# Optimization experiments

Measured on AMD Instinct MI355X. Metric: run time of the kernel, lower is better.

## Reference

```python
import jax, jax.numpy as jnp
import numpy as np

EMBED = 1024
HEADS = 16
HEAD_DIM = EMBED // HEADS
MLP = 4 * EMBED
EPS = 1e-6


def setup_inputs() -> dict:
    key = jax.random.key(0)
    ks = jax.random.split(key, 16)
    B, N, C = 2, 2048, EMBED
    x = jax.random.normal(ks[0], (B, N, C), dtype=jnp.float32)
    c = jax.random.normal(ks[1], (B, C), dtype=jnp.float32)
    attention_mask = jax.random.randint(ks[2], (B, N), 0, 2, dtype=jnp.int32)
    s = 0.02
    params = {
        "norm_w": jnp.ones((C,), jnp.float32),
        "scale_w": s * jax.random.normal(ks[3], (C, C), jnp.float32),
        "scale_b": s * jax.random.normal(ks[4], (C,), jnp.float32),
        "shift_w": s * jax.random.normal(ks[5], (C, C), jnp.float32),
        "shift_b": s * jax.random.normal(ks[6], (C,), jnp.float32),
        "qkv_w": s * jax.random.normal(ks[7], (3 * C, C), jnp.float32),
        "proj_w": s * jax.random.normal(ks[8], (C, C), jnp.float32),
        "proj_b": s * jax.random.normal(ks[9], (C,), jnp.float32),
        "mlp_w1": s * jax.random.normal(ks[10], (2 * MLP, C), jnp.float32),
        "mlp_b1": s * jax.random.normal(ks[11], (2 * MLP,), jnp.float32),
        "mlp_w2": s * jax.random.normal(ks[12], (C, MLP), jnp.float32),
        "mlp_b2": s * jax.random.normal(ks[13], (C,), jnp.float32),
    }
    return {"x": x, "c": c, "attention_mask": attention_mask, **params}


def _adaln(x, c, norm_w, scale_w, scale_b, shift_w, shift_b):
    sc = jax.nn.silu(c)
    shift = sc @ shift_w.T + shift_b                      # [B,C]
    scale = jnp.clip(sc @ scale_w.T + scale_b + 1.0, 0.1, 10.0)
    # RMSNorm: ||x|| * C^-0.5, clamped below by eps
    norm = jnp.maximum(jnp.linalg.norm(x, axis=-1, keepdims=True) * x.shape[-1] ** -0.5, EPS)
    h = x / norm * norm_w
    return h * scale[:, None, :] + shift[:, None, :]


def _attention(x, attention_mask, qkv_w, proj_w, proj_b):
    B, N, C = x.shape
    qkv = (x @ qkv_w.T).reshape(B, N, 3, HEADS, HEAD_DIM)
    q = qkv[:, :, 0].transpose(0, 2, 1, 3)  # [B,H,N,D]
    k = qkv[:, :, 1].transpose(0, 2, 1, 3)
    v = qkv[:, :, 2].transpose(0, 2, 1, 3)
    attn = jnp.einsum("bhnd,bhmd->bhnm", q, k) * (HEAD_DIM ** -0.5)
    mask = attention_mask[:, None, None, :]              # [B,1,1,N] over keys
    attn = jnp.where(mask == 0, -jnp.inf, attn)
    all_inf = jnp.all(attn == -jnp.inf, axis=-1, keepdims=True)
    attn = jnp.where(all_inf, 0.0, attn)
    p = jax.nn.softmax(attn, axis=-1)
    out = jnp.einsum("bhnm,bhmd->bhnd", p, v).transpose(0, 2, 1, 3).reshape(B, N, C)
    return out @ proj_w.T + proj_b


def _mlp(x, w1, b1, w2, b2):
    h = x @ w1.T + b1
    x1, x2 = jnp.split(h, 2, axis=-1)
    return (jax.nn.silu(x1) * x2) @ w2.T + b2


def reference(x, c, attention_mask, norm_w, scale_w, scale_b, shift_w, shift_b,
              qkv_w, proj_w, proj_b, mlp_w1, mlp_b1, mlp_w2, mlp_b2):
    x = x + _attention(_adaln(x, c, norm_w, scale_w, scale_b, shift_w, shift_b),
                       attention_mask, qkv_w, proj_w, proj_b)
    x = x + _mlp(_adaln(x, c, norm_w, scale_w, scale_b, shift_w, shift_b),
                 mlp_w1, mlp_b1, mlp_w2, mlp_b2)
    return x
```

## Files before the change

### kernel.cpp

```cpp
#include <hip/hip_runtime.h>
#include <cstdint>
#include <cstddef>

#define DEVINL __device__ __forceinline__

typedef __bf16 bf16x8 __attribute__((ext_vector_type(8)));
typedef float  f32x4  __attribute__((ext_vector_type(4)));


DEVINL unsigned short f2b(float f) {
  unsigned u = __builtin_bit_cast(unsigned, f);
  u += 0x7fffu + ((u >> 16) & 1u);
  return (unsigned short)(u >> 16);
}

DEVINL unsigned packtrunc(float a, float b) {
  unsigned ua = __builtin_bit_cast(unsigned, a);
  unsigned ub = __builtin_bit_cast(unsigned, b);
  return (ua >> 16) | (ub & 0xffff0000u);
}

DEVINL void async16(void* lds, const void* g) {
  __builtin_amdgcn_global_load_lds((const __attribute__((address_space(1))) unsigned*)g,
                                   (__attribute__((address_space(3))) unsigned*)lds,
                                   16, 0, 0);
}


__global__ void cvt4_kernel(const float* __restrict__ s0, const float* __restrict__ s1,
                            const float* __restrict__ s2, const float* __restrict__ s3,
                            unsigned short* __restrict__ d0, unsigned short* __restrict__ d1,
                            unsigned short* __restrict__ d2, unsigned short* __restrict__ d3) {
  int i = blockIdx.x * 256 + threadIdx.x;
  if (i < 786432) {
    float4 v = ((const float4*)s0)[i];
    ushort4 o; o.x = f2b(v.x); o.y = f2b(v.y); o.z = f2b(v.z); o.w = f2b(v.w);
    ((ushort4*)d0)[i] = o;
  } else if (i < 1048576) {
    int off = i - 786432;
    float4 v = ((const float4*)s1)[off];
    ushort4 o; o.x = f2b(v.x); o.y = f2b(v.y); o.z = f2b(v.z); o.w = f2b(v.w);
    ((ushort4*)d1)[off] = o;
  } else if (i < 3145728) {
    int off = i - 1048576;
    int row = off >> 8, col = off & 255;
    int rp = (row < 4096) ? (row << 1) : (((row - 4096) << 1) | 1);
    float4 v = ((const float4*)s2)[off];
    ushort4 o; o.x = f2b(v.x); o.y = f2b(v.y); o.z = f2b(v.z); o.w = f2b(v.w);
    ((ushort4*)d2)[rp * 256 + col] = o;
  } else {
    int off = i - 3145728;
    float4 v = ((const float4*)s3)[off];
    ushort4 o; o.x = f2b(v.x); o.y = f2b(v.y); o.z = f2b(v.z); o.w = f2b(v.w);
    ((ushort4*)d3)[off] = o;
  }
}


__global__ void cond_kernel(const float* __restrict__ c,
                            const float* __restrict__ scale_w, const float* __restrict__ scale_b,
                            const float* __restrict__ shift_w, const float* __restrict__ shift_b,
                            float* __restrict__ scale_o, float* __restrict__ shift_o) {
  __shared__ float sc[1024];
  __shared__ float red[2][4][64];
  int tid = threadIdx.x;
  int b = blockIdx.x >> 4, ch = blockIdx.x & 15;
  for (int i = tid; i < 1024; i += 256) {
    float cv = c[b * 1024 + i];
    sc[i] = cv / (1.f + __expf(-cv));
  }
  __syncthreads();
  int colidx = tid & 63, p = tid >> 6;
  int co = ch * 64 + colidx;
  float dsc = 0.f, dsh = 0.f;
  for (int i = 0; i < 256; ++i) {
    int kk = p * 256 + i;
    float s = sc[kk];
    dsc += s * scale_w[(size_t)co * 1024 + kk];
    dsh += s * shift_w[(size_t)co * 1024 + kk];
  }
  red[0][p][colidx] = dsc;
  red[1][p][colidx] = dsh;
  __syncthreads();
  if (p == 0) {
    float s4  = red[0][0][colidx] + red[0][1][colidx] + red[0][2][colidx] + red[0][3][colidx];
    float sh4 = red[1][0][colidx] + red[1][1][colidx] + red[1][2][colidx] + red[1][3][colidx];
    scale_o[b * 1024 + co] = fminf(fmaxf(s4 + scale_b[co] + 1.f, 0.1f), 10.f);
    shift_o[b * 1024 + co] = sh4 + shift_b[co];
  }
}


__global__ __launch_bounds__(256) void adaln_kernel(const float* __restrict__ x,
                                                    const float* __restrict__ norm_w,
                                                    const float* __restrict__ scale,
                                                    const float* __restrict__ shift,
                                                    unsigned short* __restrict__ h) {
  int row = blockIdx.x;
  int b = row >> 11;
  int tid = threadIdx.x;
  float4 v = ((const float4*)(x + (size_t)row * 1024))[tid];
  float ss = v.x * v.x + v.y * v.y + v.z * v.z + v.w * v.w;
  #pragma unroll
  for (int d = 32; d; d >>= 1) ss += __shfl_xor(ss, d);
  __shared__ float wsum[4];
  if ((tid & 63) == 0) wsum[tid >> 6] = ss;
  __syncthreads();
  float tot = wsum[0] + wsum[1] + wsum[2] + wsum[3];
  float inv = 1.f / fmaxf(sqrtf(tot * (1.f / 1024.f)), 1e-6f);
  float4 nw  = ((const float4*)norm_w)[tid];
  float4 scv = ((const float4*)(scale + b * 1024))[tid];
  float4 shv = ((const float4*)(shift + b * 1024))[tid];
  ushort4 o;
  o.x = f2b(v.x * inv * nw.x * scv.x + shv.x);
  o.y = f2b(v.y * inv * nw.y * scv.y + shv.y);
  o.z = f2b(v.z * inv * nw.z * scv.z + shv.z);
  o.w = f2b(v.w * inv * nw.w * scv.w + shv.w);
  ((ushort4*)(h + (size_t)row * 1024))[tid] = o;
}


template<int EPI, int MT>
__global__ __launch_bounds__(256, 1) void gemm_k(
    const unsigned short* __restrict__ A,
    const unsigned short* __restrict__ B0,
    const float* __restrict__ bias0,
    const float* __restrict__ resid,
    void* __restrict__ out0_, void* __restrict__ out1_, void* __restrict__ out2_,
    int M, int N, int K) {
  constexpr int MI = MT / 32;
  constexpr int A_SH = MT * 32;
  constexpr int COMPUTE_SH = 2 * A_SH + 2 * 4096;
  constexpr int STAGE_SH = (EPI == 1) ? 128 * 136 : (EPI == 2 ? 128 * 72 : 0);
  constexpr int SMEM_SH = (COMPUTE_SH > STAGE_SH) ? COMPUTE_SH : STAGE_SH;
  __shared__ __align__(16) unsigned short smem[SMEM_SH];
  unsigned short* As0 = smem;
  unsigned short* As1 = smem + A_SH;
  unsigned short* Bs0 = smem + 2 * A_SH;
  unsigned short* Bs1 = smem + 2 * A_SH + 4096;

  const int tid = threadIdx.x;
  const int wave = tid >> 6, lane = tid & 63;
  const int quad = lane >> 4, l16 = lane & 15;
  const int wm = (wave >> 1) * (MT / 2), wn = (wave & 1) * 64;
  const int bm = blockIdx.y * MT, bn = blockIdx.x * 128;

  f32x4 acc[MI][4] = {};

  const int steps = K >> 6;
  for (int s = 0; s < steps; ++s) {
    const int k0 = s << 6;
    __syncthreads();
    #pragma unroll
    for (int i = 0; i < MT / 64; ++i) {
      int cc = i * 256 + tid;
      int r = cc >> 2, ko = (cc & 3) << 3;
      size_t ga = (size_t)(bm + r) * K + k0 + ko;
      async16(As0 + (i * 2048 + wave * 512), A + ga);
      async16(As1 + (i * 2048 + wave * 512), A + ga + 32);
    }
    #pragma unroll
    for (int i = 0; i < 2; ++i) {
      int cc = i * 256 + tid;
      int r = cc >> 2, ko = (cc & 3) << 3;
      size_t gb = (size_t)(bn + r) * K + k0 + ko;
      async16(Bs0 + (i * 2048 + wave * 512), B0 + gb);
      async16(Bs1 + (i * 2048 + wave * 512), B0 + gb + 32);
    }
    __syncthreads();
    #pragma unroll
    for (int ks = 0; ks < 2; ++ks) {
      const unsigned short* Ah = ks ? As1 : As0;
      const unsigned short* Bh = ks ? Bs1 : Bs0;
      bf16x8 af[MI], bfr[4];
      #pragma unroll
      for (int mi = 0; mi < MI; ++mi)
        af[mi] = *reinterpret_cast<const bf16x8*>(&Ah[(wm + mi * 16 + l16) * 32 + quad * 8]);
      #pragma unroll
      for (int ni = 0; ni < 4; ++ni)
        bfr[ni] = *reinterpret_cast<const bf16x8*>(&Bh[(wn + ni * 16 + l16) * 32 + quad * 8]);
      #pragma unroll
      for (int mi = 0; mi < MI; ++mi)
        #pragma unroll
        for (int ni = 0; ni < 4; ++ni)
          acc[mi][ni] = __builtin_amdgcn_mfma_f32_16x16x32_bf16(af[mi], bfr[ni], acc[mi][ni], 0, 0, 0);
    }
  }

  if constexpr (EPI == 0) {
    #pragma unroll
    for (int mi = 0; mi < MI; ++mi) {
      #pragma unroll
      for (int ni = 0; ni < 4; ++ni) {
        int gc = bn + wn + ni * 16 + l16;
        #pragma unroll
        for (int r = 0; r < 4; ++r) {
          int gr = bm + wm + mi * 16 + quad * 4 + r;
          ((float*)out0_)[(size_t)gr * N + gc] = acc[mi][ni][r] + bias0[gc] + resid[(size_t)gr * N + gc];
        }
      }
    }
  } else if constexpr (EPI == 1) {
    const int region = bn >> 10;
    __syncthreads();
    #pragma unroll
    for (int mi = 0; mi < MI; ++mi) {
      #pragma unroll
      for (int ni = 0; ni < 4; ++ni) {
        int lc = wn + ni * 16 + l16;
        #pragma unroll
        for (int r = 0; r < 4; ++r) {
          int lr = wm + mi * 16 + quad * 4 + r;
          float v = acc[mi][ni][r];
          if (region == 0)      smem[lr * 136 + lc] = f2b(v * 0.125f);
          else if (region == 1) smem[lr * 136 + lc] = f2b(v);
          else                  smem[lc * 136 + lr] = f2b(v);
        }
      }
    }
    __syncthreads();
    const int b = bm >> 11;
    const int bnm = bn & 1023;
    if (region <= 1) {
      int lr = tid >> 1, hl = tid & 1;
      int n = (bm + lr) & 2047;
      int hh = (bnm >> 6) + hl;
      unsigned short* dst = (unsigned short*)(region == 0 ? out0_ : out1_) +
                            (((size_t)(b * 16 + hh)) * 2048 + n) * 64;
      const unsigned short* src = smem + lr * 136 + hl * 64;
      #pragma unroll
      for (int j = 0; j < 8; ++j)
        ((uint4*)dst)[j] = *(const uint4*)(src + j * 8);
    } else {
      int lc = tid >> 1, nh = tid & 1;
      int c2 = bnm + lc;
      int hh = c2 >> 6, d = c2 & 63;
      int nbase = (bm & 2047) + nh * 64;
      unsigned short* dst = (unsigned short*)out2_ +
                            (((size_t)(b * 16 + hh)) * 64 + d) * 2048 + nbase;
      const unsigned short* src = smem + lc * 136 + nh * 64;
      #pragma unroll
      for (int j = 0; j < 8; ++j)
        ((uint4*)dst)[j] = *(const uint4*)(src + j * 8);
    }
  } else {
    __syncthreads();
    #pragma unroll
    for (int mi = 0; mi < MI; ++mi) {
      #pragma unroll
      for (int ni = 0; ni < 4; ++ni) {
        int lc = wn + ni * 16 + l16;
        int gcp = bn + lc;
        int gi = gcp >> 1;
        float bias = bias0[(gcp & 1) ? 4096 + gi : gi];
        #pragma unroll
        for (int r = 0; r < 4; ++r) {
          int lr = wm + mi * 16 + quad * 4 + r;
          float v = acc[mi][ni][r] + bias;
          float p = __shfl_xor(v, 1);
          if ((l16 & 1) == 0) {
            float g = (v / (1.f + __expf(-v))) * p;
            smem[lr * 72 + (lc >> 1)] = f2b(g);
          }
        }
      }
    }
    __syncthreads();
    int lr = tid >> 1, ch = (tid & 1) * 32;
    unsigned short* dst = (unsigned short*)out0_ + (size_t)(bm + lr) * (N >> 1) + (bn >> 1) + ch;
    const unsigned short* src = smem + lr * 72 + ch;
    #pragma unroll
    for (int j = 0; j < 4; ++j)
      ((uint4*)dst)[j] = *(const uint4*)(src + j * 8);
  }
}


__global__ __launch_bounds__(256, 1) void attn_kernel(
    const unsigned short* __restrict__ q, const unsigned short* __restrict__ k,
    const unsigned short* __restrict__ vt, const int* __restrict__ amask,
    unsigned short* __restrict__ o) {
  const int bh = blockIdx.x;
  const int b = bh >> 4, h = bh & 15;
  const int qt = blockIdx.y;
  const int tid = threadIdx.x;
  const int wave = tid >> 6, lane = tid & 63;
  const int quad = lane >> 4, l16 = lane & 15;
  const int h7 = l16 & 7;
  const int kc0 = (quad ^ h7) * 8;
  const int kc1 = ((quad + 4) ^ h7) * 8;

  const unsigned short* qb = q  + (size_t)bh * 2048 * 64;
  const unsigned short* kb = k  + (size_t)bh * 2048 * 64;
  const unsigned short* vb = vt + (size_t)bh * 64 * 2048;

  __shared__ __align__(16) unsigned short Ks[64 * 64];
  __shared__ __align__(16) unsigned short Vs[64 * 64];
  __shared__ __align__(16) unsigned short Ps[4 * 2 * 16 * 72];
  __shared__ float biasf[64];

  unsigned short* Psm[2] = { Ps + wave * 2304, Ps + wave * 2304 + 1152 };

  bf16x8 qa[2][2];
  #pragma unroll
  for (int m = 0; m < 2; ++m) {
    int qrow = qt * 128 + wave * 32 + m * 16 + l16;
    qa[m][0] = *reinterpret_cast<const bf16x8*>(&qb[(size_t)qrow * 64 + quad * 8]);
    qa[m][1] = *reinterpret_cast<const bf16x8*>(&qb[(size_t)qrow * 64 + 32 + quad * 8]);
  }

  f32x4 oacc[2][4] = {};
  float mrow[2] = {-30000.f, -30000.f}, lrow[2] = {0.f, 0.f};

  uint4 kpre[2], vpre[2];
  #pragma unroll
  for (int i = 0; i < 2; ++i) {
    int cc = i * 256 + tid;
    int key = cc >> 3, dl = (cc & 7) ^ (key & 7);
    kpre[i] = *(const uint4*)(kb + key * 64 + dl * 8);
    int d = cc >> 3, kl = (cc & 7) ^ (d & 7);
    vpre[i] = *(const uint4*)(vb + (size_t)d * 2048 + kl * 8);
  }
  int mv = (tid < 64) ? amask[b * 2048 + tid] : 0;

  for (int kt = 0; kt < 32; ++kt) {
    __syncthreads();
    ((uint4*)Ks)[tid]       = kpre[0];
    ((uint4*)Ks)[256 + tid] = kpre[1];
    ((uint4*)Vs)[tid]       = vpre[0];
    ((uint4*)Vs)[256 + tid] = vpre[1];
    if (tid < 64) biasf[tid] = mv ? 0.f : -30000.f;
    __syncthreads();

    if (kt + 1 < 32) {
      #pragma unroll
      for (int i = 0; i < 2; ++i) {
        int cc = i * 256 + tid;
        int key = cc >> 3, dl = (cc & 7) ^ (key & 7);
        kpre[i] = *(const uint4*)(kb + (size_t)(kt + 1) * 4096 + key * 64 + dl * 8);
        int d = cc >> 3, kl = (cc & 7) ^ (d & 7);
        vpre[i] = *(const uint4*)(vb + (size_t)d * 2048 + (kt + 1) * 64 + kl * 8);
      }
      mv = (tid < 64) ? amask[b * 2048 + (kt + 1) * 64 + tid] : 0;
    }

    f32x4 st[2][4];
    #pragma unroll
    for (int nt = 0; nt < 4; ++nt) {
      bf16x8 ka0 = *reinterpret_cast<const bf16x8*>(&Ks[(nt * 16 + l16) * 64 + kc0]);
      bf16x8 ka1 = *reinterpret_cast<const bf16x8*>(&Ks[(nt * 16 + l16) * 64 + kc1]);
      f32x4 bv = *reinterpret_cast<const f32x4*>(&biasf[nt * 16 + quad * 4]);
      #pragma unroll
      for (int m = 0; m < 2; ++m) {
        f32x4 z = {};
        z = __builtin_amdgcn_mfma_f32_16x16x32_bf16(ka0, qa[m][0], z, 0, 0, 0);
        z = __builtin_amdgcn_mfma_f32_16x16x32_bf16(ka1, qa[m][1], z, 0, 0, 0);
        st[m][nt] = z + bv;
      }
    }

    #pragma unroll
    for (int m = 0; m < 2; ++m) {
      float tm = -1e30f;
      #pragma unroll
      for (int nt = 0; nt < 4; ++nt)
        #pragma unroll
        for (int r = 0; r < 4; ++r) tm = fmaxf(tm, st[m][nt][r]);
      tm = fmaxf(tm, __shfl_xor(tm, 16));
      tm = fmaxf(tm, __shfl_xor(tm, 32));

      float mnew = fmaxf(mrow[m], tm);
      float alpha = __expf(mrow[m] - mnew);
      mrow[m] = mnew;

      float rs = 0.f;
      #pragma unroll
      for (int nt = 0; nt < 4; ++nt) {
        float p0 = __expf(st[m][nt][0] - mnew);
        float p1 = __expf(st[m][nt][1] - mnew);
        float p2 = __expf(st[m][nt][2] - mnew);
        float p3 = __expf(st[m][nt][3] - mnew);
        rs += (p0 + p1) + (p2 + p3);
        uint2 w;
        w.x = packtrunc(p0, p1);
        w.y = packtrunc(p2, p3);
        *(uint2*)&Psm[m][l16 * 72 + nt * 16 + quad * 4] = w;
      }
      rs += __shfl_xor(rs, 16);
      rs += __shfl_xor(rs, 32);
      lrow[m] = lrow[m] * alpha + rs;

      float a0 = __shfl(alpha, quad * 4 + 0);
      float a1 = __shfl(alpha, quad * 4 + 1);
      float a2 = __shfl(alpha, quad * 4 + 2);
      float a3 = __shfl(alpha, quad * 4 + 3);
      #pragma unroll
      for (int dt = 0; dt < 4; ++dt) {
        oacc[m][dt][0] *= a0; oacc[m][dt][1] *= a1;
        oacc[m][dt][2] *= a2; oacc[m][dt][3] *= a3;
      }
    }

    bf16x8 pa[2][2];
    #pragma unroll
    for (int m = 0; m < 2; ++m) {
      pa[m][0] = *reinterpret_cast<const bf16x8*>(&Psm[m][l16 * 72 + quad * 8]);
      pa[m][1] = *reinterpret_cast<const bf16x8*>(&Psm[m][l16 * 72 + 32 + quad * 8]);
    }
    #pragma unroll
    for (int dt = 0; dt < 4; ++dt) {
      bf16x8 vb0 = *reinterpret_cast<const bf16x8*>(&Vs[(dt * 16 + l16) * 64 + kc0]);
      bf16x8 vb1 = *reinterpret_cast<const bf16x8*>(&Vs[(dt * 16 + l16) * 64 + kc1]);
      #pragma unroll
      for (int m = 0; m < 2; ++m) {
        oacc[m][dt] = __builtin_amdgcn_mfma_f32_16x16x32_bf16(pa[m][0], vb0, oacc[m][dt], 0, 0, 0);
        oacc[m][dt] = __builtin_amdgcn_mfma_f32_16x16x32_bf16(pa[m][1], vb1, oacc[m][dt], 0, 0, 0);
      }
    }
  }

  float iv[2][4];
  #pragma unroll
  for (int m = 0; m < 2; ++m) {
    float invl = lrow[m] > 0.f ? 1.f / lrow[m] : 0.f;
    #pragma unroll
    for (int r = 0; r < 4; ++r) iv[m][r] = __shfl(invl, quad * 4 + r);
  }
  __syncthreads();
  #pragma unroll
  for (int m = 0; m < 2; ++m)
    #pragma unroll
    for (int dt = 0; dt < 4; ++dt)
      #pragma unroll
      for (int r = 0; r < 4; ++r) {
        int lr = wave * 32 + m * 16 + quad * 4 + r;
        Ps[lr * 72 + dt * 16 + l16] = f2b(oacc[m][dt][r] * iv[m][r]);
      }
  __syncthreads();
  {
    int lr = tid >> 1, cb = (tid & 1) * 32;
    int n = qt * 128 + lr;
    unsigned short* dst = o + ((size_t)(b * 2048 + n)) * 1024 + h * 64 + cb;
    const unsigned short* src = Ps + lr * 72 + cb;
    #pragma unroll
    for (int j = 0; j < 4; ++j)
      ((uint4*)dst)[j] = *(const uint4*)(src + j * 8);
  }
}


extern "C" void kernel_launch(void* const* d_in, const int* in_sizes, int n_in,
                              void* d_out, int out_size, void* d_ws, size_t ws_size,
                              hipStream_t stream) {
  const float* x       = (const float*)d_in[0];
  const float* c       = (const float*)d_in[1];
  const int*   amask   = (const int*)d_in[2];
  const float* norm_w  = (const float*)d_in[3];
  const float* scale_w = (const float*)d_in[4];
  const float* scale_b = (const float*)d_in[5];
  const float* shift_w = (const float*)d_in[6];
  const float* shift_b = (const float*)d_in[7];
  const float* qkv_w   = (const float*)d_in[8];
  const float* proj_w  = (const float*)d_in[9];
  const float* proj_b  = (const float*)d_in[10];
  const float* mlp_w1  = (const float*)d_in[11];
  const float* mlp_b1  = (const float*)d_in[12];
  const float* mlp_w2  = (const float*)d_in[13];
  const float* mlp_b2  = (const float*)d_in[14];

  char* ws = (char*)d_ws;
  unsigned short* wqkv  = (unsigned short*)(ws + 0);
  unsigned short* wproj = (unsigned short*)(ws + 6291456);
  unsigned short* wmlp1 = (unsigned short*)(ws + 8388608);
  unsigned short* wmlp2 = (unsigned short*)(ws + 25165824);
  float* scale_o        = (float*)(ws + 33554432);
  float* shift_o        = (float*)(ws + 33562624);
  unsigned short* hbuf  = (unsigned short*)(ws + 33570816);
  unsigned short* qbuf  = (unsigned short*)(ws + 41959424);
  unsigned short* kbuf  = (unsigned short*)(ws + 50348032);
  unsigned short* vbuf  = (unsigned short*)(ws + 58736640);
  unsigned short* abuf  = (unsigned short*)(ws + 67125248);
  unsigned short* gbuf  = qbuf;
  float* x1             = (float*)(ws + 75513856);

  cvt4_kernel<<<16384, 256, 0, stream>>>(qkv_w, proj_w, mlp_w1, mlp_w2,
                                         wqkv, wproj, wmlp1, wmlp2);

  cond_kernel<<<32, 256, 0, stream>>>(c, scale_w, scale_b, shift_w, shift_b, scale_o, shift_o);

  adaln_kernel<<<4096, 256, 0, stream>>>(x, norm_w, scale_o, shift_o, hbuf);

  gemm_k<1, 128><<<dim3(24, 32), 256, 0, stream>>>(hbuf, wqkv, nullptr, nullptr,
                                                   qbuf, kbuf, vbuf, 4096, 3072, 1024);

  attn_kernel<<<dim3(32, 16), 256, 0, stream>>>(qbuf, kbuf, vbuf, amask, abuf);

  gemm_k<0, 64><<<dim3(8, 64), 256, 0, stream>>>(abuf, wproj, proj_b, x,
                                                 x1, nullptr, nullptr, 4096, 1024, 1024);

  adaln_kernel<<<4096, 256, 0, stream>>>(x1, norm_w, scale_o, shift_o, hbuf);

  gemm_k<2, 128><<<dim3(64, 32), 256, 0, stream>>>(hbuf, wmlp1, mlp_b1, nullptr,
                                                   gbuf, nullptr, nullptr, 4096, 8192, 1024);

  gemm_k<0, 64><<<dim3(8, 64), 256, 0, stream>>>(gbuf, wmlp2, mlp_b2, x1,
                                                 d_out, nullptr, nullptr, 4096, 1024, 4096);

  (void)in_sizes; (void)n_in; (void)out_size; (void)ws_size;
}
```

Measured before the change: 506.5 us.

## Split attention block across 8 waves with one 16-row query tile each

```diff
diff --git a/kernel.cpp b/kernel.cpp
--- a/kernel.cpp
+++ b/kernel.cpp
@@ -276,7 +276,7 @@
 }
 
 
-__global__ __launch_bounds__(256, 1) void attn_kernel(
+__global__ __launch_bounds__(512, 1) void attn_kernel(
     const unsigned short* __restrict__ q, const unsigned short* __restrict__ k,
     const unsigned short* __restrict__ vt, const int* __restrict__ amask,
     unsigned short* __restrict__ o) {
@@ -296,155 +296,125 @@
 
   __shared__ __align__(16) unsigned short Ks[64 * 64];
   __shared__ __align__(16) unsigned short Vs[64 * 64];
-  __shared__ __align__(16) unsigned short Ps[4 * 2 * 16 * 72];
+  __shared__ __align__(16) unsigned short Ps[8 * 16 * 72];
   __shared__ float biasf[64];
 
-  unsigned short* Psm[2] = { Ps + wave * 2304, Ps + wave * 2304 + 1152 };
-
-  bf16x8 qa[2][2];
-  #pragma unroll
-  for (int m = 0; m < 2; ++m) {
-    int qrow = qt * 128 + wave * 32 + m * 16 + l16;
-    qa[m][0] = *reinterpret_cast<const bf16x8*>(&qb[(size_t)qrow * 64 + quad * 8]);
-    qa[m][1] = *reinterpret_cast<const bf16x8*>(&qb[(size_t)qrow * 64 + 32 + quad * 8]);
-  }
-
-  f32x4 oacc[2][4] = {};
-  float mrow[2] = {-30000.f, -30000.f}, lrow[2] = {0.f, 0.f};
-
-  uint4 kpre[2], vpre[2];
-  #pragma unroll
-  for (int i = 0; i < 2; ++i) {
-    int cc = i * 256 + tid;
-    int key = cc >> 3, dl = (cc & 7) ^ (key & 7);
-    kpre[i] = *(const uint4*)(kb + key * 64 + dl * 8);
-    int d = cc >> 3, kl = (cc & 7) ^ (d & 7);
-    vpre[i] = *(const uint4*)(vb + (size_t)d * 2048 + kl * 8);
+  unsigned short* PsW = Ps + wave * 1152;
+
+  const int qrow = qt * 128 + wave * 16 + l16;
+  bf16x8 qa0 = *reinterpret_cast<const bf16x8*>(&qb[(size_t)qrow * 64 + quad * 8]);
+  bf16x8 qa1 = *reinterpret_cast<const bf16x8*>(&qb[(size_t)qrow * 64 + 32 + quad * 8]);
+
+  f32x4 oacc[4] = {};
+  float mrow = -30000.f, lrow = 0.f;
+
+  uint4 kpre, vpre;
+  {
+    int key = tid >> 3, dl = (tid & 7) ^ (key & 7);
+    kpre = *(const uint4*)(kb + key * 64 + dl * 8);
+    int d = tid >> 3, kl = (tid & 7) ^ (d & 7);
+    vpre = *(const uint4*)(vb + (size_t)d * 2048 + kl * 8);
   }
   int mv = (tid < 64) ? amask[b * 2048 + tid] : 0;
 
   for (int kt = 0; kt < 32; ++kt) {
     __syncthreads();
-    ((uint4*)Ks)[tid]       = kpre[0];
-    ((uint4*)Ks)[256 + tid] = kpre[1];
-    ((uint4*)Vs)[tid]       = vpre[0];
-    ((uint4*)Vs)[256 + tid] = vpre[1];
+    ((uint4*)Ks)[tid] = kpre;
+    ((uint4*)Vs)[tid] = vpre;
     if (tid < 64) biasf[tid] = mv ? 0.f : -30000.f;
     __syncthreads();
 
     if (kt + 1 < 32) {
-      #pragma unroll
-      for (int i = 0; i < 2; ++i) {
-        int cc = i * 256 + tid;
-        int key = cc >> 3, dl = (cc & 7) ^ (key & 7);
-        kpre[i] = *(const uint4*)(kb + (size_t)(kt + 1) * 4096 + key * 64 + dl * 8);
-        int d = cc >> 3, kl = (cc & 7) ^ (d & 7);
-        vpre[i] = *(const uint4*)(vb + (size_t)d * 2048 + (kt + 1) * 64 + kl * 8);
-      }
+      int key = tid >> 3, dl = (tid & 7) ^ (key & 7);
+      kpre = *(const uint4*)(kb + (size_t)(kt + 1) * 4096 + key * 64 + dl * 8);
+      int d = tid >> 3, kl = (tid & 7) ^ (d & 7);
+      vpre = *(const uint4*)(vb + (size_t)d * 2048 + (kt + 1) * 64 + kl * 8);
       mv = (tid < 64) ? amask[b * 2048 + (kt + 1) * 64 + tid] : 0;
     }
 
-    f32x4 st[2][4];
+    f32x4 st[4];
     #pragma unroll
     for (int nt = 0; nt < 4; ++nt) {
       bf16x8 ka0 = *reinterpret_cast<const bf16x8*>(&Ks[(nt * 16 + l16) * 64 + kc0]);
       bf16x8 ka1 = *reinterpret_cast<const bf16x8*>(&Ks[(nt * 16 + l16) * 64 + kc1]);
       f32x4 bv = *reinterpret_cast<const f32x4*>(&biasf[nt * 16 + quad * 4]);
-      #pragma unroll
-      for (int m = 0; m < 2; ++m) {
-        f32x4 z = {};
-        z = __builtin_amdgcn_mfma_f32_16x16x32_bf16(ka0, qa[m][0], z, 0, 0, 0);
-        z = __builtin_amdgcn_mfma_f32_16x16x32_bf16(ka1, qa[m][1], z, 0, 0, 0);
-        st[m][nt] = z + bv;
-      }
-    }
-
-    #pragma unroll
-    for (int m = 0; m < 2; ++m) {
-      float tm = -1e30f;
-      #pragma unroll
-      for (int nt = 0; nt < 4; ++nt)
-        #pragma unroll
-        for (int r = 0; r < 4; ++r) tm = fmaxf(tm, st[m][nt][r]);
-      tm = fmaxf(tm, __shfl_xor(tm, 16));
-      tm = fmaxf(tm, __shfl_xor(tm, 32));
-
-      float mnew = fmaxf(mrow[m], tm);
-      float alpha = __expf(mrow[m] - mnew);
-      mrow[m] = mnew;
-
-      float rs = 0.f;
-      #pragma unroll
-      for (int nt = 0; nt < 4; ++nt) {
-        float p0 = __expf(st[m][nt][0] - mnew);
-        float p1 = __expf(st[m][nt][1] - mnew);
-        float p2 = __expf(st[m][nt][2] - mnew);
-        float p3 = __expf(st[m][nt][3] - mnew);
-        rs += (p0 + p1) + (p2 + p3);
-        uint2 w;
-        w.x = packtrunc(p0, p1);
-        w.y = packtrunc(p2, p3);
-        *(uint2*)&Psm[m][l16 * 72 + nt * 16 + quad * 4] = w;
-      }
-      rs += __shfl_xor(rs, 16);
-      rs += __shfl_xor(rs, 32);
-      lrow[m] = lrow[m] * alpha + rs;
-
-      float a0 = __shfl(alpha, quad * 4 + 0);
-      float a1 = __shfl(alpha, quad * 4 + 1);
-      float a2 = __shfl(alpha, quad * 4 + 2);
-      float a3 = __shfl(alpha, quad * 4 + 3);
-      #pragma unroll
-      for (int dt = 0; dt < 4; ++dt) {
-        oacc[m][dt][0] *= a0; oacc[m][dt][1] *= a1;
-        oacc[m][dt][2] *= a2; oacc[m][dt][3] *= a3;
-      }
-    }
-
-    bf16x8 pa[2][2];
-    #pragma unroll
-    for (int m = 0; m < 2; ++m) {
-      pa[m][0] = *reinterpret_cast<const bf16x8*>(&Psm[m][l16 * 72 + quad * 8]);
-      pa[m][1] = *reinterpret_cast<const bf16x8*>(&Psm[m][l16 * 72 + 32 + quad * 8]);
-    }
+      f32x4 z = {};
+      z = __builtin_amdgcn_mfma_f32_16x16x32_bf16(ka0, qa0, z, 0, 0, 0);
+      z = __builtin_amdgcn_mfma_f32_16x16x32_bf16(ka1, qa1, z, 0, 0, 0);
+      st[nt] = z + bv;
+    }
+
+    float tm = -1e30f;
+    #pragma unroll
+    for (int nt = 0; nt < 4; ++nt)
+      #pragma unroll
+      for (int r = 0; r < 4; ++r) tm = fmaxf(tm, st[nt][r]);
+    tm = fmaxf(tm, __shfl_xor(tm, 16));
+    tm = fmaxf(tm, __shfl_xor(tm, 32));
+
+    float mnew = fmaxf(mrow, tm);
+    float alpha = __expf(mrow - mnew);
+    mrow = mnew;
+
+    float rs = 0.f;
+    #pragma unroll
+    for (int nt = 0; nt < 4; ++nt) {
+      float p0 = __expf(st[nt][0] - mnew);
+      float p1 = __expf(st[nt][1] - mnew);
+      float p2 = __expf(st[nt][2] - mnew);
+      float p3 = __expf(st[nt][3] - mnew);
+      rs += (p0 + p1) + (p2 + p3);
+      uint2 w;
+      w.x = packtrunc(p0, p1);
+      w.y = packtrunc(p2, p3);
+      *(uint2*)&PsW[l16 * 72 + nt * 16 + quad * 4] = w;
+    }
+    rs += __shfl_xor(rs, 16);
+    rs += __shfl_xor(rs, 32);
+    lrow = lrow * alpha + rs;
+
+    float a0 = __shfl(alpha, quad * 4 + 0);
+    float a1 = __shfl(alpha, quad * 4 + 1);
+    float a2 = __shfl(alpha, quad * 4 + 2);
+    float a3 = __shfl(alpha, quad * 4 + 3);
+    #pragma unroll
+    for (int dt = 0; dt < 4; ++dt) {
+      oacc[dt][0] *= a0; oacc[dt][1] *= a1; oacc[dt][2] *= a2; oacc[dt][3] *= a3;
+    }
+
+    bf16x8 pa0 = *reinterpret_cast<const bf16x8*>(&PsW[l16 * 72 + quad * 8]);
+    bf16x8 pa1 = *reinterpret_cast<const bf16x8*>(&PsW[l16 * 72 + 32 + quad * 8]);
     #pragma unroll
     for (int dt = 0; dt < 4; ++dt) {
       bf16x8 vb0 = *reinterpret_cast<const bf16x8*>(&Vs[(dt * 16 + l16) * 64 + kc0]);
       bf16x8 vb1 = *reinterpret_cast<const bf16x8*>(&Vs[(dt * 16 + l16) * 64 + kc1]);
-      #pragma unroll
-      for (int m = 0; m < 2; ++m) {
-        oacc[m][dt] = __builtin_amdgcn_mfma_f32_16x16x32_bf16(pa[m][0], vb0, oacc[m][dt], 0, 0, 0);
-        oacc[m][dt] = __builtin_amdgcn_mfma_f32_16x16x32_bf16(pa[m][1], vb1, oacc[m][dt], 0, 0, 0);
-      }
-    }
-  }
-
-  float iv[2][4];
-  #pragma unroll
-  for (int m = 0; m < 2; ++m) {
-    float invl = lrow[m] > 0.f ? 1.f / lrow[m] : 0.f;
-    #pragma unroll
-    for (int r = 0; r < 4; ++r) iv[m][r] = __shfl(invl, quad * 4 + r);
-  }
+      oacc[dt] = __builtin_amdgcn_mfma_f32_16x16x32_bf16(pa0, vb0, oacc[dt], 0, 0, 0);
+      oacc[dt] = __builtin_amdgcn_mfma_f32_16x16x32_bf16(pa1, vb1, oacc[dt], 0, 0, 0);
+    }
+  }
+
+  float invl = lrow > 0.f ? 1.f / lrow : 0.f;
+  float i0 = __shfl(invl, quad * 4 + 0);
+  float i1 = __shfl(invl, quad * 4 + 1);
+  float i2 = __shfl(invl, quad * 4 + 2);
+  float i3 = __shfl(invl, quad * 4 + 3);
   __syncthreads();
   #pragma unroll
-  for (int m = 0; m < 2; ++m)
-    #pragma unroll
-    for (int dt = 0; dt < 4; ++dt)
-      #pragma unroll
-      for (int r = 0; r < 4; ++r) {
-        int lr = wave * 32 + m * 16 + quad * 4 + r;
-        Ps[lr * 72 + dt * 16 + l16] = f2b(oacc[m][dt][r] * iv[m][r]);
-      }
+  for (int dt = 0; dt < 4; ++dt) {
+    int lr = wave * 16 + quad * 4;
+    Ps[(lr + 0) * 72 + dt * 16 + l16] = f2b(oacc[dt][0] * i0);
+    Ps[(lr + 1) * 72 + dt * 16 + l16] = f2b(oacc[dt][1] * i1);
+    Ps[(lr + 2) * 72 + dt * 16 + l16] = f2b(oacc[dt][2] * i2);
+    Ps[(lr + 3) * 72 + dt * 16 + l16] = f2b(oacc[dt][3] * i3);
+  }
   __syncthreads();
   {
-    int lr = tid >> 1, cb = (tid & 1) * 32;
+    int lr = tid >> 2, cb = (tid & 3) * 16;
     int n = qt * 128 + lr;
     unsigned short* dst = o + ((size_t)(b * 2048 + n)) * 1024 + h * 64 + cb;
     const unsigned short* src = Ps + lr * 72 + cb;
-    #pragma unroll
-    for (int j = 0; j < 4; ++j)
-      ((uint4*)dst)[j] = *(const uint4*)(src + j * 8);
+    ((uint4*)dst)[0] = *(const uint4*)(src);
+    ((uint4*)dst)[1] = *(const uint4*)(src + 8);
   }
 }
 
@@ -493,7 +463,7 @@
   gemm_k<1, 128><<<dim3(24, 32), 256, 0, stream>>>(hbuf, wqkv, nullptr, nullptr,
                                                    qbuf, kbuf, vbuf, 4096, 3072, 1024);
 
-  attn_kernel<<<dim3(32, 16), 256, 0, stream>>>(qbuf, kbuf, vbuf, amask, abuf);
+  attn_kernel<<<dim3(32, 16), 512, 0, stream>>>(qbuf, kbuf, vbuf, amask, abuf);
 
   gemm_k<0, 64><<<dim3(8, 64), 256, 0, stream>>>(abuf, wproj, proj_b, x,
                                                  x1, nullptr, nullptr, 4096, 1024, 1024);
```

Result: faster. 479.5 us (-5.3%).
